# Optimization experiments

Hardware: AMD Instinct MI355X
Metric: run time of the kernel (lower is better)

The kernel has to match this reference:

```python
import jax, jax.numpy as jnp
import numpy as np

RNN = 512
ENC = 512
HID = 512
ATT_SIZE = 196
B = 1024


def setup_inputs() -> dict:
    key = jax.random.key(0)
    ks = jax.random.split(key, 20)
    s = 0.02
    d = {
        "h": jax.random.normal(ks[0], (B, RNN), jnp.float32),
        "sentinel": jax.random.normal(ks[1], (B, RNN), jnp.float32),
        "att_feats": jax.random.normal(ks[2], (B, ATT_SIZE, RNN), jnp.float32),
        "W_ctx2att": jax.random.normal(ks[3], (RNN, HID), jnp.float32) * s,
        "b_ctx2att": jnp.zeros((HID,), jnp.float32),
        "W_sl": jax.random.normal(ks[4], (RNN, ENC), jnp.float32) * s,
        "b_sl": jnp.zeros((ENC,), jnp.float32),
        "W_se": jax.random.normal(ks[5], (ENC, HID), jnp.float32) * s,
        "b_se": jnp.zeros((HID,), jnp.float32),
        "W_hl": jax.random.normal(ks[6], (RNN, ENC), jnp.float32) * s,
        "b_hl": jnp.zeros((ENC,), jnp.float32),
        "W_he": jax.random.normal(ks[7], (ENC, HID), jnp.float32) * s,
        "b_he": jnp.zeros((HID,), jnp.float32),
        "W_alpha": jax.random.normal(ks[8], (HID, 1), jnp.float32) * s,
        "b_alpha": jnp.zeros((1,), jnp.float32),
        "W_att2h": jax.random.normal(ks[9], (RNN, RNN), jnp.float32) * s,
        "b_att2h": jnp.zeros((RNN,), jnp.float32),
    }
    return d


def reference(h, sentinel, att_feats, W_ctx2att, b_ctx2att, W_sl, b_sl,
              W_se, b_se, W_hl, b_hl, W_he, b_he, W_alpha, b_alpha,
              W_att2h, b_att2h):
    # Eval mode: dropout is identity.
    # Project attention features: [B, 196, HID]
    p_att = jnp.einsum("bsd,dh->bsh", att_feats, W_ctx2att) + b_ctx2att
    # Sentinel branch
    sent_lin = jax.nn.relu(sentinel @ W_sl + b_sl)          # [B, ENC]
    sent_emb = sent_lin @ W_se + b_se                       # [B, HID]
    # Hidden-state branch
    h_lin = jnp.tanh(h @ W_hl + b_hl)                       # [B, ENC]
    h_emb = h_lin @ W_he + b_he                             # [B, HID]
    # Concat sentinel with visual features: [B, 197, *]
    img_all = jnp.concatenate([sent_lin[:, None, :], att_feats], axis=1)
    img_all_embed = jnp.concatenate([sent_emb[:, None, :], p_att], axis=1)
    # Additive attention scores over 197 positions
    hA = jnp.tanh(img_all_embed + h_emb[:, None, :])        # [B, 197, HID]
    scores = (jnp.einsum("bsh,ho->bso", hA, W_alpha) + b_alpha)[..., 0]  # [B, 197]
    alpha = jax.nn.softmax(scores, axis=-1)
    # Weighted context
    cHat = jnp.einsum("bs,bsd->bd", alpha, img_all)          # [B, RNN]
    atten_out = cHat + h_lin
    out = jnp.tanh(atten_out @ W_att2h + b_att2h)            # [B, RNN]
    return out
```

## Files before the change

kernel.cpp:

```cpp
#include <hip/hip_runtime.h>
#include <hip/hip_bf16.h>

#define KDIM 512
#define NDIM 512
#define ATT  196
#define NB   1024

typedef __attribute__((ext_vector_type(8))) short bf16x8;
typedef __attribute__((ext_vector_type(8))) unsigned short ushort8;
typedef __attribute__((ext_vector_type(4))) float f32x4;

typedef const __attribute__((address_space(1))) unsigned int gas_uint;
typedef __attribute__((address_space(3))) unsigned int las_uint;

__device__ __forceinline__ void gload16(const void* g, void* l) {
    __builtin_amdgcn_global_load_lds((gas_uint*)g, (las_uint*)l, 16, 0, 0);
}

__device__ __forceinline__ float fast_tanh(float x) {
    x = fminf(15.f, fmaxf(-15.f, x));
    float t = __expf(2.f * x);
    return (t - 1.f) / (t + 1.f);
}

__device__ __forceinline__ unsigned short f2bf(float x) {
    union { float f; unsigned u; } v; v.f = x;
    unsigned r = v.u + 0x7FFF + ((v.u >> 16) & 1);
    return (unsigned short)(r >> 16);
}

__device__ __forceinline__ unsigned pk2(float a, float b) {
    __hip_bfloat162 h = __float22bfloat162_rn(float2{a, b});
    union { __hip_bfloat162 h2; unsigned u; } c; c.h2 = h;
    return c.u;
}

__global__ __launch_bounds__(256) void prep_weights(
        const float* __restrict__ W0, const float* __restrict__ W1,
        const float* __restrict__ W2, const float* __restrict__ W3,
        const float* __restrict__ W4, const float* __restrict__ W5,
        unsigned short* __restrict__ Wt) {
    int w = blockIdx.x >> 6;
    int t = blockIdx.x & 63;
    int k0 = (t >> 3) << 6, n0 = (t & 7) << 6;
    const float* W = (w == 0) ? W0 : (w == 1) ? W1 : (w == 2) ? W2 :
                     (w == 3) ? W3 : (w == 4) ? W4 : W5;
    __shared__ float tile[64][65];
    int tid = threadIdx.x;
    int nc = tid & 15, kr = tid >> 4;
#pragma unroll
    for (int i = 0; i < 4; ++i) {
        int k = kr + i * 16;
        float4 v = *(const float4*)&W[(size_t)(k0 + k) * NDIM + n0 + nc * 4];
        tile[k][nc * 4 + 0] = v.x; tile[k][nc * 4 + 1] = v.y;
        tile[k][nc * 4 + 2] = v.z; tile[k][nc * 4 + 3] = v.w;
    }
    __syncthreads();
    int n = tid >> 2, ks = tid & 3;
    ushort8 v0, v1;
#pragma unroll
    for (int j = 0; j < 8; ++j) v0[j] = f2bf(tile[ks * 16 + j][n]);
#pragma unroll
    for (int j = 0; j < 8; ++j) v1[j] = f2bf(tile[ks * 16 + 8 + j][n]);
    size_t base = ((size_t)w << 18) + (size_t)(n0 + n) * KDIM + k0 + ks * 16;
    *(ushort8*)&Wt[base] = v0;
    *(ushort8*)&Wt[base + 8] = v1;
}

__global__ __launch_bounds__(256) void gemm64(
        const float* __restrict__ A0, const unsigned short* __restrict__ W0,
        const float* __restrict__ bia0, float* __restrict__ O0, int act0,
        const float* __restrict__ A1, const unsigned short* __restrict__ W1,
        const float* __restrict__ bia1, float* __restrict__ O1, int act1) {
    const int op = blockIdx.y;
    const float* A = op ? A1 : A0;
    const unsigned short* Bt = op ? W1 : W0;
    const float* bias = op ? bia1 : bia0;
    float* out = op ? O1 : O0;
    const int act = op ? act1 : act0;

    __shared__ unsigned short A_lds[2][64 * 32];
    __shared__ unsigned short B_lds[2][128 * 32];

    const int tid = threadIdx.x;
    const int gm0 = (blockIdx.x >> 2) * 64, gn0 = (blockIdx.x & 3) * 128;
    const int wid = tid >> 6, lane = tid & 63;
    const int wm = wid >> 1, wn = wid & 1;
    const int lr = lane & 15, lk = lane >> 4;

    const int arow = tid >> 2, akc = tid & 3;
    const float* aptr = A + (size_t)(gm0 + arow) * KDIM + akc * 8;
    const int aoff = arow * 32 + ((akc ^ ((arow >> 1) & 3)) << 3);

    auto stageB = [&](int kt, int buf) {
#pragma unroll
        for (int j = 0; j < 2; ++j) {
            int c = tid + j * 256;
            int col = c >> 2, slot = c & 3;
            const unsigned short* src = Bt + (size_t)(gn0 + col) * KDIM +
                                        ((slot ^ ((col >> 1) & 3)) << 3) + kt * 32;
            gload16(src, &B_lds[buf][c * 8]);
        }
    };

    f32x4 acc[2][4] = {};

    {
        float4 x0 = *(const float4*)aptr;
        float4 x1 = *(const float4*)(aptr + 4);
        stageB(0, 0);
        uint4 p;
        p.x = pk2(x0.x, x0.y); p.y = pk2(x0.z, x0.w);
        p.z = pk2(x1.x, x1.y); p.w = pk2(x1.z, x1.w);
        *(uint4*)&A_lds[0][aoff] = p;
    }
    __syncthreads();

    const int swk = ((lk ^ ((lr >> 1) & 3)) << 3);
    for (int kt = 0; kt < 16; ++kt) {
        const int buf = kt & 1;
        float4 x0, x1;
        if (kt < 15) {
            const float* ap = aptr + (kt + 1) * 32;
            x0 = *(const float4*)ap;
            x1 = *(const float4*)(ap + 4);
            stageB(kt + 1, buf ^ 1);
        }
        bf16x8 af[2], bfr[4];
#pragma unroll
        for (int m = 0; m < 2; ++m)
            af[m] = *(const bf16x8*)&A_lds[buf][(wm * 32 + m * 16 + lr) * 32 + swk];
#pragma unroll
        for (int n = 0; n < 4; ++n)
            bfr[n] = *(const bf16x8*)&B_lds[buf][(wn * 64 + n * 16 + lr) * 32 + swk];
#pragma unroll
        for (int m = 0; m < 2; ++m)
#pragma unroll
            for (int n = 0; n < 4; ++n)
                acc[m][n] = __builtin_amdgcn_mfma_f32_16x16x32_bf16(af[m], bfr[n], acc[m][n], 0, 0, 0);
        if (kt < 15) {
            uint4 p;
            p.x = pk2(x0.x, x0.y); p.y = pk2(x0.z, x0.w);
            p.z = pk2(x1.x, x1.y); p.w = pk2(x1.z, x1.w);
            *(uint4*)&A_lds[buf ^ 1][aoff] = p;
        }
        __syncthreads();
    }

#pragma unroll
    for (int m = 0; m < 2; ++m)
#pragma unroll
        for (int n = 0; n < 4; ++n) {
            int col = gn0 + wn * 64 + n * 16 + lr;
            float bsv = bias[col];
#pragma unroll
            for (int r = 0; r < 4; ++r) {
                int row = gm0 + wm * 32 + m * 16 + lk * 4 + r;
                float v = acc[m][n][r] + bsv;
                if (act == 0) v = fmaxf(v, 0.f);
                else if (act == 1) v = fast_tanh(v);
                out[(size_t)row * NDIM + col] = v;
            }
        }
}

__launch_bounds__(256, 3)
__global__ void gemm_score(const float* __restrict__ A,
                           const unsigned short* __restrict__ Bt,
                           const float* __restrict__ b_ctx,
                           const float* __restrict__ h_emb,
                           const float* __restrict__ Walpha,
                           float* __restrict__ score) {
    __shared__ float A_f[2][128 * 32];
    __shared__ unsigned short B_lds[2][128 * 32];
    __shared__ float ch_s[2][128];
    __shared__ float wa_s[128];
    __shared__ float s_red[2][128];

    const int tid  = threadIdx.x;
    const int bidx = blockIdx.x;
    const int xcd  = bidx & 7, u = bidx >> 3;
    const int mblk = xcd * 196 + (u >> 2), nblk = u & 3;
    const int gm0  = mblk * 128, gn0 = nblk * 128;

    const int wid = tid >> 6, lane = tid & 63;
    const int wm  = wid >> 1, wn = wid & 1;
    const int lr  = lane & 15, lk = lane >> 4;

    const int bb0 = gm0 / ATT;
    {
        int j = tid >> 7, cloc = tid & 127;
        int bb = bb0 + j; if (bb > NB - 1) bb = NB - 1;
        ch_s[j][cloc] = b_ctx[gn0 + cloc] + h_emb[(size_t)bb * NDIM + gn0 + cloc];
        if (tid < 128) wa_s[tid] = Walpha[gn0 + tid];
    }

    const float* asrc[4];
#pragma unroll
    for (int i = 0; i < 4; ++i) {
        int c = tid + i * 256;
        int row = c >> 3, g = c & 7;
        int srcg = g ^ (row & 7);
        asrc[i] = A + (size_t)(gm0 + row) * KDIM + srcg * 4;
    }
    auto stageA = [&](int kt, int buf) {
#pragma unroll
        for (int i = 0; i < 4; ++i)
            gload16(asrc[i] + kt * 32, &A_f[buf][(tid + i * 256) * 4]);
    };

    const int c1 = tid + 256;
    const int bcol0 = tid >> 2, bk0 = (tid & 3) ^ ((bcol0 >> 1) & 3);
    const int bcol1 = c1 >> 2,  bk1 = (c1 & 3) ^ ((bcol1 >> 1) & 3);
    const unsigned short* bsrc0 = Bt + (size_t)(gn0 + bcol0) * KDIM + bk0 * 8;
    const unsigned short* bsrc1 = Bt + (size_t)(gn0 + bcol1) * KDIM + bk1 * 8;
    auto stageB = [&](int kt, int buf) {
        gload16(bsrc0 + kt * 32, &B_lds[buf][tid * 8]);
        gload16(bsrc1 + kt * 32, &B_lds[buf][c1 * 8]);
    };

    f32x4 acc[4][4] = {};
    const int swk = ((lk ^ ((lr >> 1) & 3)) << 3);

    const int arw = ((wm * 64 + lr) & 7);
    const int as0 = (lk * 2) ^ arw;
    const int as1 = (lk * 2 + 1) ^ arw;

    stageA(0, 0);
    stageB(0, 0);
    __syncthreads();

#pragma unroll 1
    for (int kt = 0; kt < 16; ++kt) {
        const int buf = kt & 1;
        if (kt < 15) {
            stageA(kt + 1, buf ^ 1);
            stageB(kt + 1, buf ^ 1);
        }
        bf16x8 af[4], bfr[4];
#pragma unroll
        for (int n = 0; n < 4; ++n)
            bfr[n] = *(const bf16x8*)&B_lds[buf][(wn * 64 + n * 16 + lr) * 32 + swk];
#pragma unroll
        for (int m = 0; m < 4; ++m) {
            const int rbase = (wm * 64 + m * 16 + lr) * 32;
            float4 fa = *(const float4*)&A_f[buf][rbase + as0 * 4];
            float4 fb = *(const float4*)&A_f[buf][rbase + as1 * 4];
            uint4 p;
            p.x = pk2(fa.x, fa.y); p.y = pk2(fa.z, fa.w);
            p.z = pk2(fb.x, fb.y); p.w = pk2(fb.z, fb.w);
            union { uint4 u; bf16x8 v; } cc; cc.u = p;
            af[m] = cc.v;
        }
#pragma unroll
        for (int m = 0; m < 4; ++m)
#pragma unroll
            for (int n = 0; n < 4; ++n)
                acc[m][n] = __builtin_amdgcn_mfma_f32_16x16x32_bf16(af[m], bfr[n], acc[m][n], 0, 0, 0);
        __syncthreads();
    }

    const int bsplit = (bb0 + 1) * ATT;
#pragma unroll
    for (int m = 0; m < 4; ++m) {
#pragma unroll
        for (int r = 0; r < 4; ++r) {
            int rloc = wm * 64 + m * 16 + lk * 4 + r;
            int rg = gm0 + rloc;
            int sel = (rg >= bsplit) ? 1 : 0;
            float sum = 0.f;
#pragma unroll
            for (int n = 0; n < 4; ++n) {
                int cloc = wn * 64 + n * 16 + lr;
                sum += fast_tanh(acc[m][n][r] + ch_s[sel][cloc]) * wa_s[cloc];
            }
            sum += __shfl_xor(sum, 1);
            sum += __shfl_xor(sum, 2);
            sum += __shfl_xor(sum, 4);
            sum += __shfl_xor(sum, 8);
            if (lr == 0) s_red[wn][rloc] = sum;
        }
    }
    __syncthreads();
    if (tid < 128) {
        float tot = s_red[0][tid] + s_red[1][tid];
        int rg = gm0 + tid;
        int sel = (rg >= bsplit) ? 1 : 0;
        int bb = bb0 + sel;
        atomicAdd(&score[(size_t)bb * 197 + (rg - bb * ATT) + 1], tot);
    }
}

__global__ __launch_bounds__(256) void softmax_chat(
        const float* __restrict__ score, const float* __restrict__ sent_emb,
        const float* __restrict__ h_emb, const float* __restrict__ Walpha,
        const float* __restrict__ sent_lin, const float* __restrict__ h_lin,
        const float* __restrict__ att, float* __restrict__ atten_out) {
    int b = blockIdx.x, tid = threadIdx.x;
    __shared__ float al[200];
    __shared__ float r4[4];

    float2 se = ((const float2*)(sent_emb + (size_t)b * NDIM))[tid];
    float2 he = ((const float2*)(h_emb + (size_t)b * NDIM))[tid];
    float2 wa = ((const float2*)Walpha)[tid];
    float val = fast_tanh(se.x + he.x) * wa.x + fast_tanh(se.y + he.y) * wa.y;
#pragma unroll
    for (int o = 32; o; o >>= 1) val += __shfl_xor(val, o);
    if ((tid & 63) == 0) r4[tid >> 6] = val;
    __syncthreads();
    float ssent = r4[0] + r4[1] + r4[2] + r4[3];
    __syncthreads();

    float v = -1e30f;
    if (tid < 197) v = (tid == 0) ? ssent : score[(size_t)b * 197 + tid];
    float m = v;
#pragma unroll
    for (int o = 32; o; o >>= 1) m = fmaxf(m, __shfl_xor(m, o));
    if ((tid & 63) == 0) r4[tid >> 6] = m;
    __syncthreads();
    m = fmaxf(fmaxf(r4[0], r4[1]), fmaxf(r4[2], r4[3]));
    __syncthreads();
    float e = (tid < 197) ? __expf(v - m) : 0.f;
    float s = e;
#pragma unroll
    for (int o = 32; o; o >>= 1) s += __shfl_xor(s, o);
    if ((tid & 63) == 0) r4[tid >> 6] = s;
    __syncthreads();
    s = r4[0] + r4[1] + r4[2] + r4[3];
    if (tid < 197) al[tid] = e / s;
    __syncthreads();

    const float2* af = (const float2*)(att + (size_t)b * ATT * KDIM);
    float2 a0 = ((const float2*)(sent_lin + (size_t)b * KDIM))[tid];
    float w0 = al[0];
    float2 accv; accv.x = w0 * a0.x; accv.y = w0 * a0.y;
#pragma unroll 14
    for (int ss = 0; ss < ATT; ++ss) {
        float w = al[ss + 1];
        float2 x = af[(size_t)ss * 256 + tid];
        accv.x += w * x.x; accv.y += w * x.y;
    }
    float2 hl = ((const float2*)(h_lin + (size_t)b * KDIM))[tid];
    accv.x += hl.x; accv.y += hl.y;
    ((float2*)(atten_out + (size_t)b * KDIM))[tid] = accv;
}

extern "C" void kernel_launch(void* const* d_in, const int* in_sizes, int n_in,
                              void* d_out, int out_size, void* d_ws, size_t ws_size,
                              hipStream_t stream) {
    const float* h     = (const float*)d_in[0];
    const float* sent  = (const float*)d_in[1];
    const float* att   = (const float*)d_in[2];
    const float* W_ctx = (const float*)d_in[3];
    const float* b_ctx = (const float*)d_in[4];
    const float* W_sl  = (const float*)d_in[5];
    const float* b_sl  = (const float*)d_in[6];
    const float* W_se  = (const float*)d_in[7];
    const float* b_se  = (const float*)d_in[8];
    const float* W_hl  = (const float*)d_in[9];
    const float* b_hl  = (const float*)d_in[10];
    const float* W_he  = (const float*)d_in[11];
    const float* b_he  = (const float*)d_in[12];
    const float* W_al  = (const float*)d_in[13];
    const float* W_a2h = (const float*)d_in[15];
    const float* b_a2h = (const float*)d_in[16];
    float* out = (float*)d_out;

    char* ws = (char*)d_ws;
    unsigned short* Wt = (unsigned short*)ws;
    float* sent_lin = (float*)(ws + 6u * 512 * 1024);
    float* h_lin    = sent_lin + (size_t)NB * 512;
    float* h_emb    = h_lin    + (size_t)NB * 512;
    float* sent_emb = h_emb    + (size_t)NB * 512;
    float* scorebuf = sent_emb + (size_t)NB * 512;
    float* atten    = scorebuf + (size_t)NB * 197;

    const size_t WSZ = 512 * 512;
    prep_weights<<<384, 256, 0, stream>>>(W_sl, W_hl, W_he, W_ctx, W_a2h, W_se, Wt);
    hipMemsetAsync(scorebuf, 0, (size_t)NB * 197 * sizeof(float), stream);

    gemm64<<<dim3(64, 2), 256, 0, stream>>>(
        sent, Wt + 0 * WSZ, b_sl, sent_lin, 0,
        h,    Wt + 1 * WSZ, b_hl, h_lin,    1);
    gemm64<<<dim3(64, 2), 256, 0, stream>>>(
        h_lin,    Wt + 2 * WSZ, b_he, h_emb,    2,
        sent_lin, Wt + 5 * WSZ, b_se, sent_emb, 2);

    gemm_score<<<6272, 256, 0, stream>>>(att, Wt + 3 * WSZ, b_ctx, h_emb, W_al, scorebuf);

    softmax_chat<<<NB, 256, 0, stream>>>(scorebuf, sent_emb, h_emb, W_al,
                                         sent_lin, h_lin, att, atten);

    gemm64<<<dim3(64, 1), 256, 0, stream>>>(
        atten, Wt + 4 * WSZ, b_a2h, out, 1,
        atten, Wt + 4 * WSZ, b_a2h, out, 1);
}
```

Before: 375.0 us.

## Enlarge gemm_score tile to 256 rows with 512-thread blocks and aliased LDS

Doubles the M tile of the fused attention-projection/score GEMM from 128 to 256 rows, using 8 waves per block and half as many blocks, so each bf16 B tile loaded to LDS is reused across twice as many rows. Shared memory becomes one 80KB buffer, and the epilogue arrays (ch_s, wa_s, s_red) alias the A staging area after the main loop, which needs an extra barrier. A 256-row tile can span three batch rows, so the bias/h_emb staging now covers up to three batches and the batch index is computed by division. Risks are lower occupancy from the large LDS footprint and fewer blocks per CU.

New measurement: 370.1 us. Within noise of the previous version (-1.3%).

```diff
diff --git a/kernel.cpp b/kernel.cpp
--- a/kernel.cpp
+++ b/kernel.cpp
@@ -164,65 +164,53 @@
         }
 }
 
-__launch_bounds__(256, 3)
+__launch_bounds__(512, 4)
 __global__ void gemm_score(const float* __restrict__ A,
                            const unsigned short* __restrict__ Bt,
                            const float* __restrict__ b_ctx,
                            const float* __restrict__ h_emb,
                            const float* __restrict__ Walpha,
                            float* __restrict__ score) {
-    __shared__ float A_f[2][128 * 32];
-    __shared__ unsigned short B_lds[2][128 * 32];
-    __shared__ float ch_s[2][128];
-    __shared__ float wa_s[128];
-    __shared__ float s_red[2][128];
+    __shared__ char smem[81920];
+    float (*A_f)[256 * 32] = (float (*)[256 * 32])smem;
+    unsigned short (*B_lds)[128 * 32] = (unsigned short (*)[128 * 32])(smem + 65536);
+    float* ch_s = (float*)smem;
+    float* wa_s = (float*)(smem + 1536);
+    float* s_red = (float*)(smem + 2048);
 
     const int tid  = threadIdx.x;
     const int bidx = blockIdx.x;
     const int xcd  = bidx & 7, u = bidx >> 3;
-    const int mblk = xcd * 196 + (u >> 2), nblk = u & 3;
-    const int gm0  = mblk * 128, gn0 = nblk * 128;
+    const int mblk = xcd * 98 + (u >> 2), nblk = u & 3;
+    const int gm0  = mblk * 256, gn0 = nblk * 128;
 
     const int wid = tid >> 6, lane = tid & 63;
     const int wm  = wid >> 1, wn = wid & 1;
     const int lr  = lane & 15, lk = lane >> 4;
 
-    const int bb0 = gm0 / ATT;
-    {
-        int j = tid >> 7, cloc = tid & 127;
-        int bb = bb0 + j; if (bb > NB - 1) bb = NB - 1;
-        ch_s[j][cloc] = b_ctx[gn0 + cloc] + h_emb[(size_t)bb * NDIM + gn0 + cloc];
-        if (tid < 128) wa_s[tid] = Walpha[gn0 + tid];
-    }
-
     const float* asrc[4];
 #pragma unroll
     for (int i = 0; i < 4; ++i) {
-        int c = tid + i * 256;
+        int c = tid + i * 512;
         int row = c >> 3, g = c & 7;
-        int srcg = g ^ (row & 7);
-        asrc[i] = A + (size_t)(gm0 + row) * KDIM + srcg * 4;
+        asrc[i] = A + (size_t)(gm0 + row) * KDIM + ((g ^ (row & 7)) << 2);
     }
     auto stageA = [&](int kt, int buf) {
 #pragma unroll
         for (int i = 0; i < 4; ++i)
-            gload16(asrc[i] + kt * 32, &A_f[buf][(tid + i * 256) * 4]);
+            gload16(asrc[i] + kt * 32, &A_f[buf][(tid + i * 512) * 4]);
     };
 
-    const int c1 = tid + 256;
-    const int bcol0 = tid >> 2, bk0 = (tid & 3) ^ ((bcol0 >> 1) & 3);
-    const int bcol1 = c1 >> 2,  bk1 = (c1 & 3) ^ ((bcol1 >> 1) & 3);
-    const unsigned short* bsrc0 = Bt + (size_t)(gn0 + bcol0) * KDIM + bk0 * 8;
-    const unsigned short* bsrc1 = Bt + (size_t)(gn0 + bcol1) * KDIM + bk1 * 8;
+    const int bcol = tid >> 2, bslot = tid & 3;
+    const unsigned short* bsrc = Bt + (size_t)(gn0 + bcol) * KDIM +
+                                 ((bslot ^ ((bcol >> 1) & 3)) << 3);
     auto stageB = [&](int kt, int buf) {
-        gload16(bsrc0 + kt * 32, &B_lds[buf][tid * 8]);
-        gload16(bsrc1 + kt * 32, &B_lds[buf][c1 * 8]);
+        gload16(bsrc + kt * 32, &B_lds[buf][tid * 8]);
     };
 
     f32x4 acc[4][4] = {};
     const int swk = ((lk ^ ((lr >> 1) & 3)) << 3);
-
-    const int arw = ((wm * 64 + lr) & 7);
+    const int arw = lr & 7;
     const int as0 = (lk * 2) ^ arw;
     const int as1 = (lk * 2 + 1) ^ arw;
 
@@ -260,33 +248,43 @@
         __syncthreads();
     }
 
-    const int bsplit = (bb0 + 1) * ATT;
+    const int bb0 = gm0 / ATT;
+    {
+        int j = tid >> 7;
+        int c = tid & 127;
+        if (j < 3) {
+            int bb = bb0 + j; if (bb > NB - 1) bb = NB - 1;
+            ch_s[j * 128 + c] = b_ctx[gn0 + c] + h_emb[(size_t)bb * NDIM + gn0 + c];
+        }
+        if (tid < 128) wa_s[tid] = Walpha[gn0 + tid];
+    }
+    __syncthreads();
+
 #pragma unroll
     for (int m = 0; m < 4; ++m) {
 #pragma unroll
         for (int r = 0; r < 4; ++r) {
             int rloc = wm * 64 + m * 16 + lk * 4 + r;
             int rg = gm0 + rloc;
-            int sel = (rg >= bsplit) ? 1 : 0;
+            int sel = rg / ATT - bb0;
             float sum = 0.f;
 #pragma unroll
             for (int n = 0; n < 4; ++n) {
                 int cloc = wn * 64 + n * 16 + lr;
-                sum += fast_tanh(acc[m][n][r] + ch_s[sel][cloc]) * wa_s[cloc];
+                sum += fast_tanh(acc[m][n][r] + ch_s[sel * 128 + cloc]) * wa_s[cloc];
             }
             sum += __shfl_xor(sum, 1);
             sum += __shfl_xor(sum, 2);
             sum += __shfl_xor(sum, 4);
             sum += __shfl_xor(sum, 8);
-            if (lr == 0) s_red[wn][rloc] = sum;
-        }
-    }
-    __syncthreads();
-    if (tid < 128) {
-        float tot = s_red[0][tid] + s_red[1][tid];
+            if (lr == 0) s_red[wn * 256 + rloc] = sum;
+        }
+    }
+    __syncthreads();
+    if (tid < 256) {
+        float tot = s_red[tid] + s_red[256 + tid];
         int rg = gm0 + tid;
-        int sel = (rg >= bsplit) ? 1 : 0;
-        int bb = bb0 + sel;
+        int bb = rg / ATT;
         atomicAdd(&score[(size_t)bb * 197 + (rg - bb * ATT) + 1], tot);
     }
 }
@@ -386,7 +384,7 @@
         h_lin,    Wt + 2 * WSZ, b_he, h_emb,    2,
         sent_lin, Wt + 5 * WSZ, b_se, sent_emb, 2);
 
-    gemm_score<<<6272, 256, 0, stream>>>(att, Wt + 3 * WSZ, b_ctx, h_emb, W_al, scorebuf);
+    gemm_score<<<3136, 512, 0, stream>>>(att, Wt + 3 * WSZ, b_ctx, h_emb, W_al, scorebuf);
 
     softmax_chat<<<NB, 256, 0, stream>>>(scorebuf, sent_emb, h_emb, W_al,
                                          sent_lin, h_lin, att, atten);
```

## Triple-buffer gemm_score LDS pipeline with a single barrier per k-step

Applied to the files above, without the earlier changes.

Moves the score GEMM from double to triple buffering. Tiles are prefetched two k-steps ahead, and explicit vmcnt waits plus one barrier per iteration replace the two syncthreads. MFMA issue priority is also raised with s_setprio around the matrix block. The goal is to hide global-to-LDS load latency and cut barrier stalls. In exchange, LDS use goes up and occupancy drops from 3 to 2 blocks per CU.

After: 457.0 us. +21.9%, slower.

```diff
diff --git a/kernel.cpp b/kernel.cpp
--- a/kernel.cpp
+++ b/kernel.cpp
@@ -164,15 +164,15 @@
         }
 }
 
-__launch_bounds__(256, 3)
+__launch_bounds__(256, 2)
 __global__ void gemm_score(const float* __restrict__ A,
                            const unsigned short* __restrict__ Bt,
                            const float* __restrict__ b_ctx,
                            const float* __restrict__ h_emb,
                            const float* __restrict__ Walpha,
                            float* __restrict__ score) {
-    __shared__ float A_f[2][128 * 32];
-    __shared__ unsigned short B_lds[2][128 * 32];
+    __shared__ float A_f[3][128 * 32];
+    __shared__ unsigned short B_lds[3][128 * 32];
     __shared__ float ch_s[2][128];
     __shared__ float wa_s[128];
     __shared__ float s_red[2][128];
@@ -200,8 +200,7 @@
     for (int i = 0; i < 4; ++i) {
         int c = tid + i * 256;
         int row = c >> 3, g = c & 7;
-        int srcg = g ^ (row & 7);
-        asrc[i] = A + (size_t)(gm0 + row) * KDIM + srcg * 4;
+        asrc[i] = A + (size_t)(gm0 + row) * KDIM + ((g ^ (row & 7)) << 2);
     }
     auto stageA = [&](int kt, int buf) {
 #pragma unroll
@@ -221,44 +220,56 @@
 
     f32x4 acc[4][4] = {};
     const int swk = ((lk ^ ((lr >> 1) & 3)) << 3);
-
-    const int arw = ((wm * 64 + lr) & 7);
+    const int arw = lr & 7;
     const int as0 = (lk * 2) ^ arw;
     const int as1 = (lk * 2 + 1) ^ arw;
 
-    stageA(0, 0);
-    stageB(0, 0);
-    __syncthreads();
-
+    stageA(0, 0); stageB(0, 0);
+    stageA(1, 1); stageB(1, 1);
+
+    int cur = 0;
 #pragma unroll 1
     for (int kt = 0; kt < 16; ++kt) {
-        const int buf = kt & 1;
-        if (kt < 15) {
-            stageA(kt + 1, buf ^ 1);
-            stageB(kt + 1, buf ^ 1);
-        }
+        if (kt < 15)
+            asm volatile("s_waitcnt vmcnt(6)" ::: "memory");
+        else
+            asm volatile("s_waitcnt vmcnt(0)" ::: "memory");
+        __builtin_amdgcn_sched_barrier(0);
+        __builtin_amdgcn_s_barrier();
+        __builtin_amdgcn_sched_barrier(0);
+
+        if (kt + 2 < 16) {
+            int nb = cur + 2; if (nb >= 3) nb -= 3;
+            stageA(kt + 2, nb);
+            stageB(kt + 2, nb);
+        }
+
         bf16x8 af[4], bfr[4];
 #pragma unroll
         for (int n = 0; n < 4; ++n)
-            bfr[n] = *(const bf16x8*)&B_lds[buf][(wn * 64 + n * 16 + lr) * 32 + swk];
+            bfr[n] = *(const bf16x8*)&B_lds[cur][(wn * 64 + n * 16 + lr) * 32 + swk];
 #pragma unroll
         for (int m = 0; m < 4; ++m) {
             const int rbase = (wm * 64 + m * 16 + lr) * 32;
-            float4 fa = *(const float4*)&A_f[buf][rbase + as0 * 4];
-            float4 fb = *(const float4*)&A_f[buf][rbase + as1 * 4];
+            float4 fa = *(const float4*)&A_f[cur][rbase + as0 * 4];
+            float4 fb = *(const float4*)&A_f[cur][rbase + as1 * 4];
             uint4 p;
             p.x = pk2(fa.x, fa.y); p.y = pk2(fa.z, fa.w);
             p.z = pk2(fb.x, fb.y); p.w = pk2(fb.z, fb.w);
             union { uint4 u; bf16x8 v; } cc; cc.u = p;
             af[m] = cc.v;
         }
+        __builtin_amdgcn_s_setprio(1);
 #pragma unroll
         for (int m = 0; m < 4; ++m)
 #pragma unroll
             for (int n = 0; n < 4; ++n)
                 acc[m][n] = __builtin_amdgcn_mfma_f32_16x16x32_bf16(af[m], bfr[n], acc[m][n], 0, 0, 0);
-        __syncthreads();
-    }
+        __builtin_amdgcn_s_setprio(0);
+
+        cur = (cur == 2) ? 0 : cur + 1;
+    }
+    __syncthreads();
 
     const int bsplit = (bb0 + 1) * ATT;
 #pragma unroll
```
